# Kernel tuning notes

Measured on AMD Instinct MI355X. Metric: run time of the kernel, lower is better.

The kernel has to match this reference:

```python
import jax, jax.numpy as jnp
import numpy as np

B, S, D_MODEL, FFN, P = 8, 4096, 256, 1024, 8
BLK = 256  # token block size for the max-plus reduction


def setup_inputs() -> dict:
    key = jax.random.key(0)
    ks = jax.random.split(key, 12)
    x = jax.random.normal(ks[0], (B, S, D_MODEL), jnp.float32)
    # TropicalLinear params (additive semiring weights -> small scale)
    Wt = 0.05 * jax.random.normal(ks[1], (FFN, D_MODEL), jnp.float32)
    bt = 0.05 * jax.random.normal(ks[2], (FFN,), jnp.float32)
    # LFDualActivation: per-channel piecewise-linear convex (max) and concave (min)
    # branches, blended by a per-channel sigmoid gate alpha ('blend' mode).
    sl_cvx = 1.0 + 0.1 * jax.random.normal(ks[3], (FFN, P), jnp.float32)
    of_cvx = 0.1 * jax.random.normal(ks[4], (FFN, P), jnp.float32)
    sl_ccv = 1.0 + 0.1 * jax.random.normal(ks[5], (FFN, P), jnp.float32)
    of_ccv = 0.1 * jax.random.normal(ks[6], (FFN, P), jnp.float32)
    alpha = jnp.zeros((FFN,), jnp.float32)
    # Classical branch
    Wc = jax.random.normal(ks[7], (D_MODEL, FFN), jnp.float32) / np.sqrt(D_MODEL)
    bc = jnp.zeros((FFN,), jnp.float32)
    # Gate: init per source (weight ~0, bias +2.0 -> g ~ 0.88 tropical)
    Wg = 0.01 * jax.random.normal(ks[8], (D_MODEL, FFN), jnp.float32)
    bg = 2.0 * jnp.ones((FFN,), jnp.float32)
    # Down projection
    Wd = jax.random.normal(ks[9], (FFN, D_MODEL), jnp.float32) / np.sqrt(FFN)
    bd = jnp.zeros((D_MODEL,), jnp.float32)
    return {"x": x, "Wt": Wt, "bt": bt, "sl_cvx": sl_cvx, "of_cvx": of_cvx,
            "sl_ccv": sl_ccv, "of_ccv": of_ccv, "alpha": alpha,
            "Wc": Wc, "bc": bc, "Wg": Wg, "bg": bg, "Wd": Wd, "bd": bd}


def reference(x, Wt, bt, sl_cvx, of_cvx, sl_ccv, of_ccv, alpha, Wc, bc, Wg, bg, Wd, bd):
    Bx, Sx, D = x.shape
    T = Bx * Sx
    xf = x.reshape(T, D)
    xb = xf.reshape(T // BLK, BLK, D)
    s = jax.nn.sigmoid(alpha)  # [FFN]

    def blk_fn(xx):  # xx: [BLK, D]
        # Tropical (max-plus) linear: t[n,m] = max_k(xx[n,k] + Wt[m,k]) + bt[m]
        t = jnp.max(xx[:, None, :] + Wt[None, :, :], axis=-1) + bt  # [BLK, FFN]
        # LF dual activation: blend of convex (max of lines) and concave (min of lines)
        z = t[:, :, None]  # [BLK, FFN, 1]
        cvx = jnp.max(z * sl_cvx[None] + of_cvx[None], axis=-1)
        ccv = jnp.min(z * sl_ccv[None] + of_ccv[None], axis=-1)
        return s * cvx + (1.0 - s) * ccv  # [BLK, FFN]

    trop = jax.lax.map(blk_fn, xb).reshape(T, FFN)  # dropout = identity (eval)
    classical = jax.nn.gelu(xf @ Wc + bc, approximate=False)
    g = jax.nn.sigmoid(xf @ Wg + bg)
    fused = g * trop + (1.0 - g) * classical
    out = fused @ Wd + bd  # final dropout = identity (eval)
    return out.reshape(Bx, Sx, D)
```

## Files before the change

kernel.cpp:

```cpp
#include <hip/hip_runtime.h>

#define TTOK 32768
#define DM   256
#define NF   1024
#define KMAX 32

typedef __attribute__((ext_vector_type(8))) unsigned short ushort8;
typedef __attribute__((ext_vector_type(8))) __bf16 bf16x8;
typedef __attribute__((ext_vector_type(4))) float floatx4;

constexpr size_t O_SLOT = 0;
constexpr size_t O_S    = 256;
constexpr size_t O_WCT  = O_S    + 4096;
constexpr size_t O_WGT  = O_WCT  + (size_t)NF*DM*2;
constexpr size_t O_WDT  = O_WGT  + (size_t)NF*DM*2;
constexpr size_t O_WTT  = O_WDT  + (size_t)DM*NF*2;
constexpr size_t O_XBF  = O_WTT  + (size_t)DM*NF*4;
constexpr size_t O_CNT  = O_XBF  + (size_t)TTOK*DM*2;
constexpr size_t O_CIDX = O_CNT  + (size_t)TTOK*4;
constexpr size_t O_CVAL = O_CIDX + (size_t)TTOK*KMAX*4;
constexpr size_t O_FUSD = O_CVAL + (size_t)TTOK*KMAX*4;

__device__ __forceinline__ float bf2f(unsigned short u) {
    union { unsigned int i; float f; } c; c.i = ((unsigned int)u) << 16; return c.f;
}
__device__ __forceinline__ unsigned short f2bf(float v) {
    union { float f; unsigned int i; } c; c.f = v;
    unsigned int b = c.i;
    return (unsigned short)((b + 0x7FFFu + ((b >> 16) & 1u)) >> 16);
}
__device__ __forceinline__ float sigm(float z) { return 1.0f / (1.0f + __expf(-z)); }
__device__ __forceinline__ float gelu_f(float x) {
    return x * sigm(1.59576912f * (x + 0.044715f * x * x * x));
}
__device__ __forceinline__ void g2lds16(const unsigned short* g, unsigned short* l) {
    __builtin_amdgcn_global_load_lds((const __attribute__((address_space(1))) unsigned int*)g,
                                     (__attribute__((address_space(3))) unsigned int*)l, 16, 0, 0);
}

__global__ void pack_kernel(const float* __restrict__ Wt, const float* __restrict__ alpha,
                            const float* __restrict__ Wc, const float* __restrict__ Wg,
                            const float* __restrict__ Wd,
                            unsigned short* __restrict__ Wct, unsigned short* __restrict__ Wgt,
                            unsigned short* __restrict__ WdT, float* __restrict__ WtT,
                            float* __restrict__ s, unsigned int* __restrict__ slot) {
    int e = blockIdx.x * 256 + threadIdx.x;
    if (e == 0) *slot = 0u;
    { int f = e >> 8, k = e & 255;
      Wct[e] = f2bf(Wc[k * NF + f]);
      Wgt[e] = f2bf(Wg[k * NF + f]); }
    { int n = e >> 10, k = e & 1023;
      WdT[e] = f2bf(Wd[k * DM + n]); }
    { int d = e >> 10, f = e & 1023;
      WtT[e] = Wt[f * DM + d]; }
    if (e < NF) s[e] = sigm(alpha[e]);
}

__global__ void minmax_kernel(const float* __restrict__ Wt, unsigned int* __restrict__ slot) {
    int g = blockIdx.x * 256 + threadIdx.x;
    float lm = 0.0f;
    for (int i = g; i < NF * DM; i += 128 * 256) lm = fmaxf(lm, fabsf(Wt[i]));
    #pragma unroll
    for (int o = 32; o > 0; o >>= 1) lm = fmaxf(lm, __shfl_xor(lm, o));
    if ((threadIdx.x & 63) == 0) atomicMax(slot, __float_as_uint(lm));
}

__global__ void cand_kernel(const float* __restrict__ x, const unsigned int* __restrict__ slot,
                            unsigned short* __restrict__ xbf, int* __restrict__ counts,
                            int* __restrict__ cidx, float* __restrict__ cval) {
    int i = blockIdx.x, t = threadIdx.x;
    float v = x[i * DM + t];
    xbf[i * DM + t] = f2bf(v);
    float m = v;
    #pragma unroll
    for (int o = 32; o > 0; o >>= 1) m = fmaxf(m, __shfl_xor(m, o));
    __shared__ float wm[4];
    __shared__ int cnt;
    __shared__ int sidx[KMAX];
    __shared__ float sval[KMAX];
    if ((t & 63) == 0) wm[t >> 6] = m;
    if (t == 0) cnt = 0;
    __syncthreads();
    float xmax = fmaxf(fmaxf(wm[0], wm[1]), fmaxf(wm[2], wm[3]));
    float delta = 2.0f * __uint_as_float(*slot);
    float thr = xmax - delta;
    if (v >= thr) {
        int p = atomicAdd(&cnt, 1);
        if (p < KMAX) { sidx[p] = t; sval[p] = v; }
    }
    __syncthreads();
    int c = cnt;
    if (t == 0) counts[i] = c;
    if (t < (c < KMAX ? c : KMAX)) {
        cidx[i * KMAX + t] = sidx[t];
        cval[i * KMAX + t] = sval[t];
    }
}

#define LDSS 32
#define KPAD 33
#define OSTR 136
__global__ __launch_bounds__(512, 4) void gemm1_kernel(
    const unsigned short* __restrict__ A,
    const unsigned short* __restrict__ Bct,
    const unsigned short* __restrict__ Bgt,
    const float* __restrict__ bc, const float* __restrict__ bg,
    const int* __restrict__ counts, const int* __restrict__ cidx,
    const float* __restrict__ cval, const float* __restrict__ x,
    const float* __restrict__ WtT, const float* __restrict__ bt,
    const float* __restrict__ slx, const float* __restrict__ ofx,
    const float* __restrict__ slc, const float* __restrict__ ofc,
    const float* __restrict__ s, unsigned short* __restrict__ fused) {
    __shared__ __align__(16) char smem[76800];
    unsigned short* As  = (unsigned short*)smem;
    unsigned short* Bcs = As + 4096;
    unsigned short* Bgs = As + 8192;
    float* par = (float*)smem;
    int* sOV  = (int*)(smem + 24576);
    int* sCnt = (int*)(smem + 41472);
    unsigned short* obuf = (unsigned short*)(smem + 41984);
    const int t = threadIdx.x;
    const int b = blockIdx.x;
    const int xcd = b & 7, j = b >> 3;
    const int bf = j & 7;
    const int bm = (j >> 3) * 8 + xcd;
    const int wave = t >> 6, lane = t & 63;
    const int wm = wave & 1, wn = wave >> 1;
    const int lr = lane & 15, quad = lane >> 4;
    const int srow = wave * 16 + (lane >> 2), scol = (lane & 3) << 3;
    const unsigned short* gA = A   + (size_t)(bm * 128 + srow) * DM + scol;
    const unsigned short* gC = Bct + (size_t)(bf * 128 + srow) * DM + scol;
    const unsigned short* gG = Bgt + (size_t)(bf * 128 + srow) * DM + scol;
    unsigned short* lA = &As[wave * 16 * LDSS];
    unsigned short* lC = &Bcs[wave * 16 * LDSS];
    unsigned short* lG = &Bgs[wave * 16 * LDSS];

    if (t < 128) sCnt[t] = counts[bm * 128 + t];

    floatx4 accc[4][2], accg[4][2];
    #pragma unroll
    for (int i = 0; i < 4; i++)
        #pragma unroll
        for (int jj = 0; jj < 2; jj++) { accc[i][jj] = (floatx4)0.0f; accg[i][jj] = (floatx4)0.0f; }

    for (int k0 = 0; k0 < DM; k0 += 32) {
        __syncthreads();
        g2lds16(gA + k0, lA);
        g2lds16(gC + k0, lC);
        g2lds16(gG + k0, lG);
        __syncthreads();
        bf16x8 af[4], bcf[2], bgf[2];
        #pragma unroll
        for (int mi = 0; mi < 4; mi++)
            af[mi] = *(const bf16x8*)&As[(wm * 64 + mi * 16 + lr) * LDSS + quad * 8];
        #pragma unroll
        for (int ni = 0; ni < 2; ni++) {
            bcf[ni] = *(const bf16x8*)&Bcs[(wn * 32 + ni * 16 + lr) * LDSS + quad * 8];
            bgf[ni] = *(const bf16x8*)&Bgs[(wn * 32 + ni * 16 + lr) * LDSS + quad * 8];
        }
        #pragma unroll
        for (int mi = 0; mi < 4; mi++)
            #pragma unroll
            for (int ni = 0; ni < 2; ni++) {
                accc[mi][ni] = __builtin_amdgcn_mfma_f32_16x16x32_bf16(af[mi], bcf[ni], accc[mi][ni], 0, 0, 0);
                accg[mi][ni] = __builtin_amdgcn_mfma_f32_16x16x32_bf16(af[mi], bgf[ni], accg[mi][ni], 0, 0, 0);
            }
    }
    __syncthreads();

    for (int e = t; e < 1024; e += 512) {
        int ff = e >> 3, w = e & 7;
        int gf = (bf * 128 + ff) * 8 + w;
        par[ff * 36 + w]      = slx[gf];
        par[ff * 36 + 8 + w]  = ofx[gf];
        par[ff * 36 + 16 + w] = slc[gf];
        par[ff * 36 + 24 + w] = ofc[gf];
    }
    if (t < 128) {
        int gf = bf * 128 + t;
        par[t * 36 + 32] = bt[gf];
        par[t * 36 + 33] = s[gf];
        par[t * 36 + 34] = bc[gf];
        par[t * 36 + 35] = bg[gf];
    }
    const int PADV = (int)(((unsigned int)f2bf(-1e30f)) << 16);
    for (int e = t; e < 128 * KMAX; e += 512) {
        int m = e >> 5, k = e & 31;
        int c = sCnt[m];
        int pk = PADV;
        if (k < (c < KMAX ? c : KMAX)) {
            int d  = cidx[(size_t)(bm * 128 + m) * KMAX + k];
            float v = cval[(size_t)(bm * 128 + m) * KMAX + k];
            pk = (int)(((unsigned int)f2bf(v)) << 16) | d;
        }
        sOV[m * KPAD + k] = pk;
    }
    __syncthreads();

    const int f0 = bf * 128 + wn * 32 + lr;
    #pragma unroll
    for (int mi = 0; mi < 4; mi++) {
        const int mb = wm * 64 + mi * 16 + quad * 4;
        int c0 = sCnt[mb], c1 = sCnt[mb + 1], c2 = sCnt[mb + 2], c3 = sCnt[mb + 3];
        int k0c = c0 < KMAX ? c0 : KMAX, k1c = c1 < KMAX ? c1 : KMAX;
        int k2c = c2 < KMAX ? c2 : KMAX, k3c = c3 < KMAX ? c3 : KMAX;
        int km = max(max(k0c, k1c), max(k2c, k3c));
        float z0a = -1e30f, z1a = -1e30f, z2a = -1e30f, z3a = -1e30f;
        float z0b = -1e30f, z1b = -1e30f, z2b = -1e30f, z3b = -1e30f;
        for (int k = 0; k < km; k++) {
            int p0 = sOV[(mb + 0) * KPAD + k];
            int p1 = sOV[(mb + 1) * KPAD + k];
            int p2 = sOV[(mb + 2) * KPAD + k];
            int p3 = sOV[(mb + 3) * KPAD + k];
            const float* r0 = WtT + ((p0 & 0xFFFF) << 10) + f0;
            const float* r1 = WtT + ((p1 & 0xFFFF) << 10) + f0;
            const float* r2 = WtT + ((p2 & 0xFFFF) << 10) + f0;
            const float* r3 = WtT + ((p3 & 0xFFFF) << 10) + f0;
            float w0a = r0[0], w0b = r0[16];
            float w1a = r1[0], w1b = r1[16];
            float w2a = r2[0], w2b = r2[16];
            float w3a = r3[0], w3b = r3[16];
            float v0 = __int_as_float(p0 & 0xFFFF0000);
            float v1 = __int_as_float(p1 & 0xFFFF0000);
            float v2 = __int_as_float(p2 & 0xFFFF0000);
            float v3 = __int_as_float(p3 & 0xFFFF0000);
            z0a = fmaxf(z0a, v0 + w0a); z0b = fmaxf(z0b, v0 + w0b);
            z1a = fmaxf(z1a, v1 + w1a); z1b = fmaxf(z1b, v1 + w1b);
            z2a = fmaxf(z2a, v2 + w2a); z2b = fmaxf(z2b, v2 + w2b);
            z3a = fmaxf(z3a, v3 + w3a); z3b = fmaxf(z3b, v3 + w3b);
        }
        if (c0 > KMAX || c1 > KMAX || c2 > KMAX || c3 > KMAX) {
            float za[4] = { z0a, z1a, z2a, z3a };
            float zb[4] = { z0b, z1b, z2b, z3b };
            int cc[4] = { c0, c1, c2, c3 };
            #pragma unroll 1
            for (int r = 0; r < 4; r++) if (cc[r] > KMAX) {
                const float* xr = x + (size_t)(bm * 128 + mb + r) * DM;
                float ma = -1e30f, mbv = -1e30f;
                for (int d = 0; d < DM; d++) {
                    float xv = xr[d];
                    ma  = fmaxf(ma,  xv + WtT[d * NF + f0]);
                    mbv = fmaxf(mbv, xv + WtT[d * NF + f0 + 16]);
                }
                za[r] = ma; zb[r] = mbv;
            }
            z0a = za[0]; z1a = za[1]; z2a = za[2]; z3a = za[3];
            z0b = zb[0]; z1b = zb[1]; z2b = zb[2]; z3b = zb[3];
        }
        #pragma unroll
        for (int ni = 0; ni < 2; ni++) {
            const int fl = wn * 32 + ni * 16 + lr;
            const float* pp = par + fl * 36;
            float4 a0 = *(const float4*)(pp),      a1 = *(const float4*)(pp + 4);
            float4 b0 = *(const float4*)(pp + 8),  b1 = *(const float4*)(pp + 12);
            float4 cc0 = *(const float4*)(pp + 16), cc1 = *(const float4*)(pp + 20);
            float4 d0 = *(const float4*)(pp + 24), d1 = *(const float4*)(pp + 28);
            float4 sc = *(const float4*)(pp + 32);
            float zr[4];
            if (ni == 0) { zr[0] = z0a; zr[1] = z1a; zr[2] = z2a; zr[3] = z3a; }
            else         { zr[0] = z0b; zr[1] = z1b; zr[2] = z2b; zr[3] = z3b; }
            #pragma unroll
            for (int r = 0; r < 4; r++) {
                float z = zr[r] + sc.x;
                float cvx = fmaf(z, a0.x, b0.x);
                cvx = fmaxf(cvx, fmaf(z, a0.y, b0.y));
                cvx = fmaxf(cvx, fmaf(z, a0.z, b0.z));
                cvx = fmaxf(cvx, fmaf(z, a0.w, b0.w));
                cvx = fmaxf(cvx, fmaf(z, a1.x, b1.x));
                cvx = fmaxf(cvx, fmaf(z, a1.y, b1.y));
                cvx = fmaxf(cvx, fmaf(z, a1.z, b1.z));
                cvx = fmaxf(cvx, fmaf(z, a1.w, b1.w));
                float ccv = fmaf(z, cc0.x, d0.x);
                ccv = fminf(ccv, fmaf(z, cc0.y, d0.y));
                ccv = fminf(ccv, fmaf(z, cc0.z, d0.z));
                ccv = fminf(ccv, fmaf(z, cc0.w, d0.w));
                ccv = fminf(ccv, fmaf(z, cc1.x, d1.x));
                ccv = fminf(ccv, fmaf(z, cc1.y, d1.y));
                ccv = fminf(ccv, fmaf(z, cc1.z, d1.z));
                ccv = fminf(ccv, fmaf(z, cc1.w, d1.w));
                float tv = sc.y * cvx + (1.0f - sc.y) * ccv;
                float cpre = accc[mi][ni][r] + sc.z;
                float gpre = accg[mi][ni][r] + sc.w;
                float g = sigm(gpre);
                float cla = gelu_f(cpre);
                obuf[(mb + r) * OSTR + fl] = f2bf(g * tv + (1.0f - g) * cla);
            }
        }
    }
    __syncthreads();
    #pragma unroll
    for (int e = t; e < 128 * 16; e += 512) {
        int row = e >> 4, c8 = (e & 15) << 3;
        ushort8 v = *(const ushort8*)&obuf[row * OSTR + c8];
        *(ushort8*)&fused[(size_t)(bm * 128 + row) * NF + bf * 128 + c8] = v;
    }
}

#define LDS2 64
__global__ __launch_bounds__(512, 4) void gemm2_kernel(
    const unsigned short* __restrict__ A,
    const unsigned short* __restrict__ Bt,
    const float* __restrict__ bd, float* __restrict__ out) {
    __shared__ __align__(16) unsigned short As[128 * LDS2];
    __shared__ __align__(16) unsigned short Bs[128 * LDS2];
    const int t = threadIdx.x;
    const int b = blockIdx.x;
    const int xcd = b & 7, j = b >> 3;
    const int bn = j & 1;
    const int bm = (j >> 1) * 8 + xcd;
    const int wave = t >> 6, lane = t & 63;
    const int wm = wave & 1, wn = wave >> 1;
    const int lr = lane & 15, quad = lane >> 4;
    const int srow = wave * 8 + (lane >> 3), scol = (lane & 7) << 3;
    const unsigned short* gA = A  + (size_t)(bm * 128 + srow) * NF + scol;
    const unsigned short* gB = Bt + (size_t)(bn * 128 + srow) * NF + scol;
    unsigned short* lA = &As[wave * 8 * LDS2];
    unsigned short* lB = &Bs[wave * 8 * LDS2];

    floatx4 acc[4][2];
    #pragma unroll
    for (int i = 0; i < 4; i++)
        #pragma unroll
        for (int jj = 0; jj < 2; jj++) acc[i][jj] = (floatx4)0.0f;

    for (int k0 = 0; k0 < NF; k0 += 64) {
        __syncthreads();
        g2lds16(gA + k0, lA);
        g2lds16(gA + k0 + (size_t)64 * NF, lA + 64 * LDS2);
        g2lds16(gB + k0, lB);
        g2lds16(gB + k0 + (size_t)64 * NF, lB + 64 * LDS2);
        __syncthreads();
        #pragma unroll
        for (int ks = 0; ks < 2; ks++) {
            bf16x8 af[4], bf_[2];
            #pragma unroll
            for (int mi = 0; mi < 4; mi++)
                af[mi] = *(const bf16x8*)&As[(wm * 64 + mi * 16 + lr) * LDS2 + ks * 32 + quad * 8];
            #pragma unroll
            for (int ni = 0; ni < 2; ni++)
                bf_[ni] = *(const bf16x8*)&Bs[(wn * 32 + ni * 16 + lr) * LDS2 + ks * 32 + quad * 8];
            #pragma unroll
            for (int mi = 0; mi < 4; mi++)
                #pragma unroll
                for (int ni = 0; ni < 2; ni++)
                    acc[mi][ni] = __builtin_amdgcn_mfma_f32_16x16x32_bf16(af[mi], bf_[ni], acc[mi][ni], 0, 0, 0);
        }
    }
    #pragma unroll
    for (int mi = 0; mi < 4; mi++)
        #pragma unroll
        for (int ni = 0; ni < 2; ni++) {
            int n = bn * 128 + wn * 32 + ni * 16 + lr;
            float bdv = bd[n];
            #pragma unroll
            for (int r = 0; r < 4; r++) {
                int m = bm * 128 + wm * 64 + mi * 16 + quad * 4 + r;
                out[m * DM + n] = acc[mi][ni][r] + bdv;
            }
        }
}

extern "C" void kernel_launch(void* const* d_in, const int* in_sizes, int n_in,
                              void* d_out, int out_size, void* d_ws, size_t ws_size,
                              hipStream_t stream) {
    const float* x     = (const float*)d_in[0];
    const float* Wt    = (const float*)d_in[1];
    const float* bt    = (const float*)d_in[2];
    const float* slx   = (const float*)d_in[3];
    const float* ofx   = (const float*)d_in[4];
    const float* slc   = (const float*)d_in[5];
    const float* ofc   = (const float*)d_in[6];
    const float* alpha = (const float*)d_in[7];
    const float* Wc    = (const float*)d_in[8];
    const float* bc    = (const float*)d_in[9];
    const float* Wg    = (const float*)d_in[10];
    const float* bg    = (const float*)d_in[11];
    const float* Wd    = (const float*)d_in[12];
    const float* bd    = (const float*)d_in[13];
    float* out = (float*)d_out;
    char* ws = (char*)d_ws;

    unsigned int* slot = (unsigned int*)(ws + O_SLOT);
    float* s           = (float*)(ws + O_S);
    unsigned short* Wct = (unsigned short*)(ws + O_WCT);
    unsigned short* Wgt = (unsigned short*)(ws + O_WGT);
    unsigned short* WdT = (unsigned short*)(ws + O_WDT);
    float* WtT          = (float*)(ws + O_WTT);
    unsigned short* xbf = (unsigned short*)(ws + O_XBF);
    int* counts         = (int*)(ws + O_CNT);
    int* cidx           = (int*)(ws + O_CIDX);
    float* cval         = (float*)(ws + O_CVAL);
    unsigned short* fused = (unsigned short*)(ws + O_FUSD);

    pack_kernel<<<1024, 256, 0, stream>>>(Wt, alpha, Wc, Wg, Wd, Wct, Wgt, WdT, WtT, s, slot);
    minmax_kernel<<<128, 256, 0, stream>>>(Wt, slot);
    cand_kernel<<<TTOK, 256, 0, stream>>>(x, slot, xbf, counts, cidx, cval);
    gemm1_kernel<<<2048, 512, 0, stream>>>(
        xbf, Wct, Wgt, bc, bg, counts, cidx, cval, x, WtT, bt,
        slx, ofx, slc, ofc, s, fused);
    gemm2_kernel<<<512, 512, 0, stream>>>(fused, WdT, bd, out);
}
```

Measured before the change: 286.6 us.

## Shrink gemm1 tile to 128x64, cut LDS, cap candidates, per-wave output stores

The fused first GEMM now uses 128x64 output tiles and launches twice as many blocks. Its LDS footprint drops from about 75 KB to 31 KB, and launch bounds are raised to 6 blocks per CU to get more occupancy. The candidate list kept in LDS is capped at 12 entries and loaded before the GEMM loop. Any row with more candidates falls back to the exact full max-plus scan. Output is staged per wave with an XOR swizzle and written directly, which removes the final block-wide barrier, at the cost of reloading A tiles twice as often.

```diff
diff --git a/kernel.cpp b/kernel.cpp
--- a/kernel.cpp
+++ b/kernel.cpp
@@ -97,10 +97,10 @@
     }
 }
 
-#define LDSS 32
-#define KPAD 33
-#define OSTR 136
-__global__ __launch_bounds__(512, 4) void gemm1_kernel(
+#define LDSS  32
+#define KCAP  12
+#define KPADL 13
+__global__ __launch_bounds__(512, 6) void gemm1_kernel(
     const unsigned short* __restrict__ A,
     const unsigned short* __restrict__ Bct,
     const unsigned short* __restrict__ Bgt,
@@ -111,55 +111,68 @@
     const float* __restrict__ slx, const float* __restrict__ ofx,
     const float* __restrict__ slc, const float* __restrict__ ofc,
     const float* __restrict__ s, unsigned short* __restrict__ fused) {
-    __shared__ __align__(16) char smem[76800];
+    __shared__ __align__(16) char smem[31744];
     unsigned short* As  = (unsigned short*)smem;
     unsigned short* Bcs = As + 4096;
-    unsigned short* Bgs = As + 8192;
+    unsigned short* Bgs = As + 6144;
     float* par = (float*)smem;
+    unsigned short* obuf = (unsigned short*)(smem + 16384);
     int* sOV  = (int*)(smem + 24576);
-    int* sCnt = (int*)(smem + 41472);
-    unsigned short* obuf = (unsigned short*)(smem + 41984);
+    int* sCnt = (int*)(smem + 31232);
     const int t = threadIdx.x;
     const int b = blockIdx.x;
     const int xcd = b & 7, j = b >> 3;
-    const int bf = j & 7;
-    const int bm = (j >> 3) * 8 + xcd;
+    const int bfb = j & 15;
+    const int bm  = (j >> 4) * 8 + xcd;
     const int wave = t >> 6, lane = t & 63;
-    const int wm = wave & 1, wn = wave >> 1;
+    const int wm = wave >> 1, wf = wave & 1;
     const int lr = lane & 15, quad = lane >> 4;
-    const int srow = wave * 16 + (lane >> 2), scol = (lane & 3) << 3;
-    const unsigned short* gA = A   + (size_t)(bm * 128 + srow) * DM + scol;
-    const unsigned short* gC = Bct + (size_t)(bf * 128 + srow) * DM + scol;
-    const unsigned short* gG = Bgt + (size_t)(bf * 128 + srow) * DM + scol;
-    unsigned short* lA = &As[wave * 16 * LDSS];
-    unsigned short* lC = &Bcs[wave * 16 * LDSS];
-    unsigned short* lG = &Bgs[wave * 16 * LDSS];
 
     if (t < 128) sCnt[t] = counts[bm * 128 + t];
-
-    floatx4 accc[4][2], accg[4][2];
-    #pragma unroll
-    for (int i = 0; i < 4; i++)
+    const int PADV = (int)(((unsigned int)f2bf(-1e30f)) << 16);
+    for (int e = t; e < 2048; e += 512) {
+        int m = e >> 4, k = e & 15;
+        if (k < KCAP) {
+            int c = counts[bm * 128 + m];
+            int pk = PADV;
+            if (k < (c < KCAP ? c : KCAP)) {
+                int d  = cidx[(size_t)(bm * 128 + m) * KMAX + k];
+                float v = cval[(size_t)(bm * 128 + m) * KMAX + k];
+                pk = (int)(((unsigned int)f2bf(v)) << 16) | d;
+            }
+            sOV[m * KPADL + k] = pk;
+        }
+    }
+
+    const unsigned short* gbase;
+    unsigned short* lbase;
+    if (wave < 4)      { gbase = A   + (size_t)(bm * 128 + wave * 32) * DM;       lbase = &As[wave * 32 * LDSS]; }
+    else if (wave < 6) { gbase = Bct + (size_t)(bfb * 64 + (wave - 4) * 32) * DM; lbase = &Bcs[(wave - 4) * 32 * LDSS]; }
+    else               { gbase = Bgt + (size_t)(bfb * 64 + (wave - 6) * 32) * DM; lbase = &Bgs[(wave - 6) * 32 * LDSS]; }
+    const unsigned short* g0 = gbase + (size_t)(lane >> 2) * DM + ((lane & 3) << 3);
+
+    floatx4 accc[2][2], accg[2][2];
+    #pragma unroll
+    for (int i = 0; i < 2; i++)
         #pragma unroll
         for (int jj = 0; jj < 2; jj++) { accc[i][jj] = (floatx4)0.0f; accg[i][jj] = (floatx4)0.0f; }
 
     for (int k0 = 0; k0 < DM; k0 += 32) {
         __syncthreads();
-        g2lds16(gA + k0, lA);
-        g2lds16(gC + k0, lC);
-        g2lds16(gG + k0, lG);
+        g2lds16(g0 + k0, lbase);
+        g2lds16(g0 + 16 * DM + k0, lbase + 16 * LDSS);
         __syncthreads();
-        bf16x8 af[4], bcf[2], bgf[2];
-        #pragma unroll
-        for (int mi = 0; mi < 4; mi++)
-            af[mi] = *(const bf16x8*)&As[(wm * 64 + mi * 16 + lr) * LDSS + quad * 8];
+        bf16x8 af[2], bcf[2], bgf[2];
+        #pragma unroll
+        for (int mi = 0; mi < 2; mi++)
+            af[mi] = *(const bf16x8*)&As[(wm * 32 + mi * 16 + lr) * LDSS + quad * 8];
         #pragma unroll
         for (int ni = 0; ni < 2; ni++) {
-            bcf[ni] = *(const bf16x8*)&Bcs[(wn * 32 + ni * 16 + lr) * LDSS + quad * 8];
-            bgf[ni] = *(const bf16x8*)&Bgs[(wn * 32 + ni * 16 + lr) * LDSS + quad * 8];
-        }
-        #pragma unroll
-        for (int mi = 0; mi < 4; mi++)
+            bcf[ni] = *(const bf16x8*)&Bcs[(wf * 32 + ni * 16 + lr) * LDSS + quad * 8];
+            bgf[ni] = *(const bf16x8*)&Bgs[(wf * 32 + ni * 16 + lr) * LDSS + quad * 8];
+        }
+        #pragma unroll
+        for (int mi = 0; mi < 2; mi++)
             #pragma unroll
             for (int ni = 0; ni < 2; ni++) {
                 accc[mi][ni] = __builtin_amdgcn_mfma_f32_16x16x32_bf16(af[mi], bcf[ni], accc[mi][ni], 0, 0, 0);
@@ -168,50 +181,37 @@
     }
     __syncthreads();
 
-    for (int e = t; e < 1024; e += 512) {
-        int ff = e >> 3, w = e & 7;
-        int gf = (bf * 128 + ff) * 8 + w;
-        par[ff * 36 + w]      = slx[gf];
-        par[ff * 36 + 8 + w]  = ofx[gf];
-        par[ff * 36 + 16 + w] = slc[gf];
-        par[ff * 36 + 24 + w] = ofc[gf];
-    }
-    if (t < 128) {
-        int gf = bf * 128 + t;
+    { int ff = t >> 3, w = t & 7;
+      int gf = (bfb * 64 + ff) * 8 + w;
+      par[ff * 36 + w]      = slx[gf];
+      par[ff * 36 + 8 + w]  = ofx[gf];
+      par[ff * 36 + 16 + w] = slc[gf];
+      par[ff * 36 + 24 + w] = ofc[gf]; }
+    if (t < 64) {
+        int gf = bfb * 64 + t;
         par[t * 36 + 32] = bt[gf];
         par[t * 36 + 33] = s[gf];
         par[t * 36 + 34] = bc[gf];
         par[t * 36 + 35] = bg[gf];
     }
-    const int PADV = (int)(((unsigned int)f2bf(-1e30f)) << 16);
-    for (int e = t; e < 128 * KMAX; e += 512) {
-        int m = e >> 5, k = e & 31;
-        int c = sCnt[m];
-        int pk = PADV;
-        if (k < (c < KMAX ? c : KMAX)) {
-            int d  = cidx[(size_t)(bm * 128 + m) * KMAX + k];
-            float v = cval[(size_t)(bm * 128 + m) * KMAX + k];
-            pk = (int)(((unsigned int)f2bf(v)) << 16) | d;
-        }
-        sOV[m * KPAD + k] = pk;
-    }
     __syncthreads();
 
-    const int f0 = bf * 128 + wn * 32 + lr;
-    #pragma unroll
-    for (int mi = 0; mi < 4; mi++) {
-        const int mb = wm * 64 + mi * 16 + quad * 4;
+    const int f0 = bfb * 64 + wf * 32 + lr;
+    unsigned short* owave = obuf + wave * 512;
+    #pragma unroll
+    for (int mi = 0; mi < 2; mi++) {
+        const int mb = wm * 32 + mi * 16 + quad * 4;
         int c0 = sCnt[mb], c1 = sCnt[mb + 1], c2 = sCnt[mb + 2], c3 = sCnt[mb + 3];
-        int k0c = c0 < KMAX ? c0 : KMAX, k1c = c1 < KMAX ? c1 : KMAX;
-        int k2c = c2 < KMAX ? c2 : KMAX, k3c = c3 < KMAX ? c3 : KMAX;
+        int k0c = c0 < KCAP ? c0 : KCAP, k1c = c1 < KCAP ? c1 : KCAP;
+        int k2c = c2 < KCAP ? c2 : KCAP, k3c = c3 < KCAP ? c3 : KCAP;
         int km = max(max(k0c, k1c), max(k2c, k3c));
         float z0a = -1e30f, z1a = -1e30f, z2a = -1e30f, z3a = -1e30f;
         float z0b = -1e30f, z1b = -1e30f, z2b = -1e30f, z3b = -1e30f;
         for (int k = 0; k < km; k++) {
-            int p0 = sOV[(mb + 0) * KPAD + k];
-            int p1 = sOV[(mb + 1) * KPAD + k];
-            int p2 = sOV[(mb + 2) * KPAD + k];
-            int p3 = sOV[(mb + 3) * KPAD + k];
+            int p0 = sOV[(mb + 0) * KPADL + k];
+            int p1 = sOV[(mb + 1) * KPADL + k];
+            int p2 = sOV[(mb + 2) * KPADL + k];
+            int p3 = sOV[(mb + 3) * KPADL + k];
             const float* r0 = WtT + ((p0 & 0xFFFF) << 10) + f0;
             const float* r1 = WtT + ((p1 & 0xFFFF) << 10) + f0;
             const float* r2 = WtT + ((p2 & 0xFFFF) << 10) + f0;
@@ -229,12 +229,12 @@
             z2a = fmaxf(z2a, v2 + w2a); z2b = fmaxf(z2b, v2 + w2b);
             z3a = fmaxf(z3a, v3 + w3a); z3b = fmaxf(z3b, v3 + w3b);
         }
-        if (c0 > KMAX || c1 > KMAX || c2 > KMAX || c3 > KMAX) {
+        if (c0 > KCAP || c1 > KCAP || c2 > KCAP || c3 > KCAP) {
             float za[4] = { z0a, z1a, z2a, z3a };
             float zb[4] = { z0b, z1b, z2b, z3b };
             int cc[4] = { c0, c1, c2, c3 };
             #pragma unroll 1
-            for (int r = 0; r < 4; r++) if (cc[r] > KMAX) {
+            for (int r = 0; r < 4; r++) if (cc[r] > KCAP) {
                 const float* xr = x + (size_t)(bm * 128 + mb + r) * DM;
                 float ma = -1e30f, mbv = -1e30f;
                 for (int d = 0; d < DM; d++) {
@@ -249,7 +249,7 @@
         }
         #pragma unroll
         for (int ni = 0; ni < 2; ni++) {
-            const int fl = wn * 32 + ni * 16 + lr;
+            const int fl = wf * 32 + ni * 16 + lr;
             const float* pp = par + fl * 36;
             float4 a0 = *(const float4*)(pp),      a1 = *(const float4*)(pp + 4);
             float4 b0 = *(const float4*)(pp + 8),  b1 = *(const float4*)(pp + 12);
@@ -283,16 +283,16 @@
                 float gpre = accg[mi][ni][r] + sc.w;
                 float g = sigm(gpre);
                 float cla = gelu_f(cpre);
-                obuf[(mb + r) * OSTR + fl] = f2bf(g * tv + (1.0f - g) * cla);
+                int row = quad * 4 + r;
+                owave[row * 32 + ((ni * 16 + lr) ^ (quad << 3))] = f2bf(g * tv + (1.0f - g) * cla);
             }
         }
-    }
-    __syncthreads();
-    #pragma unroll
-    for (int e = t; e < 128 * 16; e += 512) {
-        int row = e >> 4, c8 = (e & 15) << 3;
-        ushort8 v = *(const ushort8*)&obuf[row * OSTR + c8];
-        *(ushort8*)&fused[(size_t)(bm * 128 + row) * NF + bf * 128 + c8] = v;
+        {
+            int rl = lane >> 2, ch = lane & 3;
+            ushort8 v = *(const ushort8*)&owave[rl * 32 + ((ch ^ (rl >> 2)) << 3)];
+            *(ushort8*)&fused[(size_t)(bm * 128 + wm * 32 + mi * 16 + rl) * NF
+                              + bfb * 64 + wf * 32 + ch * 8] = v;
+        }
     }
 }
 
@@ -395,7 +395,7 @@
     pack_kernel<<<1024, 256, 0, stream>>>(Wt, alpha, Wc, Wg, Wd, Wct, Wgt, WdT, WtT, s, slot);
     minmax_kernel<<<128, 256, 0, stream>>>(Wt, slot);
     cand_kernel<<<TTOK, 256, 0, stream>>>(x, slot, xbf, counts, cidx, cval);
-    gemm1_kernel<<<2048, 512, 0, stream>>>(
+    gemm1_kernel<<<4096, 512, 0, stream>>>(
         xbf, Wct, Wgt, bc, bg, counts, cidx, cval, x, WtT, bt,
         slx, ofx, slc, ofc, s, fused);
     gemm2_kernel<<<512, 512, 0, stream>>>(fused, WdT, bd, out);
```

Result: slower. 495.2 us (+72.8%).

## Double-buffer GEMM1 K-loop, use wave-per-token candidate selection, cap candidates

Applied to the files above, without the earlier changes.

The candidate kernel now gives each token to a single wavefront and compacts candidates with ballot/popcount instead of shared-memory atomics and block barriers, so a launch has a quarter as many blocks. In gemm1, the shared-memory layout is reorganised so the candidate and parameter staging happens before the MFMA loop, and that loop double-buffers its LDS tiles so the next K slice loads while the current one computes. The per-token candidate cap used in gemm1 drops from 32 to 16, which sends more tokens to the slow full-scan fallback if they have many candidates.

```diff
diff --git a/kernel.cpp b/kernel.cpp
--- a/kernel.cpp
+++ b/kernel.cpp
@@ -65,41 +65,47 @@
     if ((threadIdx.x & 63) == 0) atomicMax(slot, __float_as_uint(lm));
 }
 
-__global__ void cand_kernel(const float* __restrict__ x, const unsigned int* __restrict__ slot,
-                            unsigned short* __restrict__ xbf, int* __restrict__ counts,
-                            int* __restrict__ cidx, float* __restrict__ cval) {
-    int i = blockIdx.x, t = threadIdx.x;
-    float v = x[i * DM + t];
-    xbf[i * DM + t] = f2bf(v);
-    float m = v;
+__global__ __launch_bounds__(256) void cand_kernel(
+        const float* __restrict__ x, const unsigned int* __restrict__ slot,
+        unsigned short* __restrict__ xbf, int* __restrict__ counts,
+        int* __restrict__ cidx, float* __restrict__ cval) {
+    const int wave = threadIdx.x >> 6, lane = threadIdx.x & 63;
+    const int tok = blockIdx.x * 4 + wave;
+    const float* xr = x + (size_t)tok * DM;
+    float v0 = xr[lane], v1 = xr[lane + 64], v2 = xr[lane + 128], v3 = xr[lane + 192];
+    unsigned short* xo = xbf + (size_t)tok * DM;
+    xo[lane]       = f2bf(v0);
+    xo[lane + 64]  = f2bf(v1);
+    xo[lane + 128] = f2bf(v2);
+    xo[lane + 192] = f2bf(v3);
+    float m = fmaxf(fmaxf(v0, v1), fmaxf(v2, v3));
     #pragma unroll
     for (int o = 32; o > 0; o >>= 1) m = fmaxf(m, __shfl_xor(m, o));
-    __shared__ float wm[4];
-    __shared__ int cnt;
-    __shared__ int sidx[KMAX];
-    __shared__ float sval[KMAX];
-    if ((t & 63) == 0) wm[t >> 6] = m;
-    if (t == 0) cnt = 0;
-    __syncthreads();
-    float xmax = fmaxf(fmaxf(wm[0], wm[1]), fmaxf(wm[2], wm[3]));
-    float delta = 2.0f * __uint_as_float(*slot);
-    float thr = xmax - delta;
-    if (v >= thr) {
-        int p = atomicAdd(&cnt, 1);
-        if (p < KMAX) { sidx[p] = t; sval[p] = v; }
-    }
-    __syncthreads();
-    int c = cnt;
-    if (t == 0) counts[i] = c;
-    if (t < (c < KMAX ? c : KMAX)) {
-        cidx[i * KMAX + t] = sidx[t];
-        cval[i * KMAX + t] = sval[t];
-    }
-}
-
-#define LDSS 32
-#define KPAD 33
-#define OSTR 136
+    const float delta = 2.0f * __uint_as_float(*slot);
+    const float thr = m - delta;
+    const unsigned long long lt = (lane == 63) ? 0x7FFFFFFFFFFFFFFFull
+                                               : ((1ull << lane) - 1ull);
+    float vv[4] = { v0, v1, v2, v3 };
+    int base = 0;
+    #pragma unroll
+    for (int j = 0; j < 4; j++) {
+        bool p = vv[j] >= thr;
+        unsigned long long mask = __ballot(p);
+        int pos = base + __popcll(mask & lt);
+        if (p && pos < KMAX) {
+            cidx[(size_t)tok * KMAX + pos] = lane + j * 64;
+            cval[(size_t)tok * KMAX + pos] = vv[j];
+        }
+        base += __popcll(mask);
+    }
+    if (lane == 0) counts[tok] = base;
+}
+
+#define LDSS  32
+#define KCAP  16
+#define KPADL 17
+#define OSTR  136
+#define STAGEB 24576
 __global__ __launch_bounds__(512, 4) void gemm1_kernel(
     const unsigned short* __restrict__ A,
     const unsigned short* __restrict__ Bct,
@@ -112,13 +118,10 @@
     const float* __restrict__ slc, const float* __restrict__ ofc,
     const float* __restrict__ s, unsigned short* __restrict__ fused) {
     __shared__ __align__(16) char smem[76800];
-    unsigned short* As  = (unsigned short*)smem;
-    unsigned short* Bcs = As + 4096;
-    unsigned short* Bgs = As + 8192;
-    float* par = (float*)smem;
-    int* sOV  = (int*)(smem + 24576);
-    int* sCnt = (int*)(smem + 41472);
-    unsigned short* obuf = (unsigned short*)(smem + 41984);
+    unsigned short* obuf = (unsigned short*)smem;
+    float* par = (float*)(smem + 49152);
+    int* sOV  = (int*)(smem + 67584);
+    int* sCnt = (int*)(smem + 76288);
     const int t = threadIdx.x;
     const int b = blockIdx.x;
     const int xcd = b & 7, j = b >> 3;
@@ -131,43 +134,23 @@
     const unsigned short* gA = A   + (size_t)(bm * 128 + srow) * DM + scol;
     const unsigned short* gC = Bct + (size_t)(bf * 128 + srow) * DM + scol;
     const unsigned short* gG = Bgt + (size_t)(bf * 128 + srow) * DM + scol;
-    unsigned short* lA = &As[wave * 16 * LDSS];
-    unsigned short* lC = &Bcs[wave * 16 * LDSS];
-    unsigned short* lG = &Bgs[wave * 16 * LDSS];
+    const int lofs = wave * 16 * LDSS;
 
     if (t < 128) sCnt[t] = counts[bm * 128 + t];
-
-    floatx4 accc[4][2], accg[4][2];
-    #pragma unroll
-    for (int i = 0; i < 4; i++)
-        #pragma unroll
-        for (int jj = 0; jj < 2; jj++) { accc[i][jj] = (floatx4)0.0f; accg[i][jj] = (floatx4)0.0f; }
-
-    for (int k0 = 0; k0 < DM; k0 += 32) {
-        __syncthreads();
-        g2lds16(gA + k0, lA);
-        g2lds16(gC + k0, lC);
-        g2lds16(gG + k0, lG);
-        __syncthreads();
-        bf16x8 af[4], bcf[2], bgf[2];
-        #pragma unroll
-        for (int mi = 0; mi < 4; mi++)
-            af[mi] = *(const bf16x8*)&As[(wm * 64 + mi * 16 + lr) * LDSS + quad * 8];
-        #pragma unroll
-        for (int ni = 0; ni < 2; ni++) {
-            bcf[ni] = *(const bf16x8*)&Bcs[(wn * 32 + ni * 16 + lr) * LDSS + quad * 8];
-            bgf[ni] = *(const bf16x8*)&Bgs[(wn * 32 + ni * 16 + lr) * LDSS + quad * 8];
-        }
-        #pragma unroll
-        for (int mi = 0; mi < 4; mi++)
-            #pragma unroll
-            for (int ni = 0; ni < 2; ni++) {
-                accc[mi][ni] = __builtin_amdgcn_mfma_f32_16x16x32_bf16(af[mi], bcf[ni], accc[mi][ni], 0, 0, 0);
-                accg[mi][ni] = __builtin_amdgcn_mfma_f32_16x16x32_bf16(af[mi], bgf[ni], accg[mi][ni], 0, 0, 0);
-            }
-    }
-    __syncthreads();
-
+    const int PADV = (int)(((unsigned int)f2bf(-1e30f)) << 16);
+    #pragma unroll
+    for (int e = t; e < 2048; e += 512) {
+        int m = e >> 4, k = e & 15;
+        int c = counts[bm * 128 + m];
+        int pk = PADV;
+        if (k < (c < KCAP ? c : KCAP)) {
+            int d  = cidx[(size_t)(bm * 128 + m) * KMAX + k];
+            float v = cval[(size_t)(bm * 128 + m) * KMAX + k];
+            pk = (int)(((unsigned int)f2bf(v)) << 16) | d;
+        }
+        sOV[m * KPADL + k] = pk;
+    }
+    #pragma unroll
     for (int e = t; e < 1024; e += 512) {
         int ff = e >> 3, w = e & 7;
         int gf = (bf * 128 + ff) * 8 + w;
@@ -183,35 +166,64 @@
         par[t * 36 + 34] = bc[gf];
         par[t * 36 + 35] = bg[gf];
     }
-    const int PADV = (int)(((unsigned int)f2bf(-1e30f)) << 16);
-    for (int e = t; e < 128 * KMAX; e += 512) {
-        int m = e >> 5, k = e & 31;
-        int c = sCnt[m];
-        int pk = PADV;
-        if (k < (c < KMAX ? c : KMAX)) {
-            int d  = cidx[(size_t)(bm * 128 + m) * KMAX + k];
-            float v = cval[(size_t)(bm * 128 + m) * KMAX + k];
-            pk = (int)(((unsigned int)f2bf(v)) << 16) | d;
-        }
-        sOV[m * KPAD + k] = pk;
+
+    floatx4 accc[4][2], accg[4][2];
+    #pragma unroll
+    for (int i = 0; i < 4; i++)
+        #pragma unroll
+        for (int jj = 0; jj < 2; jj++) { accc[i][jj] = (floatx4)0.0f; accg[i][jj] = (floatx4)0.0f; }
+
+    {
+        unsigned short* b0 = (unsigned short*)smem;
+        g2lds16(gA, b0 + lofs);
+        g2lds16(gC, b0 + 4096 + lofs);
+        g2lds16(gG, b0 + 8192 + lofs);
     }
     __syncthreads();
+    #pragma unroll
+    for (int k = 0; k < 8; k++) {
+        unsigned short* cur = (unsigned short*)(smem + (size_t)(k & 1) * STAGEB);
+        if (k < 7) {
+            unsigned short* nxt = (unsigned short*)(smem + (size_t)((k + 1) & 1) * STAGEB);
+            int k0 = (k + 1) * 32;
+            g2lds16(gA + k0, nxt + lofs);
+            g2lds16(gC + k0, nxt + 4096 + lofs);
+            g2lds16(gG + k0, nxt + 8192 + lofs);
+        }
+        bf16x8 af[4], bcf[2], bgf[2];
+        #pragma unroll
+        for (int mi = 0; mi < 4; mi++)
+            af[mi] = *(const bf16x8*)&cur[(wm * 64 + mi * 16 + lr) * LDSS + quad * 8];
+        #pragma unroll
+        for (int ni = 0; ni < 2; ni++) {
+            bcf[ni] = *(const bf16x8*)&cur[4096 + (wn * 32 + ni * 16 + lr) * LDSS + quad * 8];
+            bgf[ni] = *(const bf16x8*)&cur[8192 + (wn * 32 + ni * 16 + lr) * LDSS + quad * 8];
+        }
+        #pragma unroll
+        for (int mi = 0; mi < 4; mi++)
+            #pragma unroll
+            for (int ni = 0; ni < 2; ni++) {
+                accc[mi][ni] = __builtin_amdgcn_mfma_f32_16x16x32_bf16(af[mi], bcf[ni], accc[mi][ni], 0, 0, 0);
+                accg[mi][ni] = __builtin_amdgcn_mfma_f32_16x16x32_bf16(af[mi], bgf[ni], accg[mi][ni], 0, 0, 0);
+            }
+        __syncthreads();
+    }
 
     const int f0 = bf * 128 + wn * 32 + lr;
     #pragma unroll
     for (int mi = 0; mi < 4; mi++) {
         const int mb = wm * 64 + mi * 16 + quad * 4;
         int c0 = sCnt[mb], c1 = sCnt[mb + 1], c2 = sCnt[mb + 2], c3 = sCnt[mb + 3];
-        int k0c = c0 < KMAX ? c0 : KMAX, k1c = c1 < KMAX ? c1 : KMAX;
-        int k2c = c2 < KMAX ? c2 : KMAX, k3c = c3 < KMAX ? c3 : KMAX;
+        int k0c = c0 < KCAP ? c0 : KCAP, k1c = c1 < KCAP ? c1 : KCAP;
+        int k2c = c2 < KCAP ? c2 : KCAP, k3c = c3 < KCAP ? c3 : KCAP;
         int km = max(max(k0c, k1c), max(k2c, k3c));
         float z0a = -1e30f, z1a = -1e30f, z2a = -1e30f, z3a = -1e30f;
         float z0b = -1e30f, z1b = -1e30f, z2b = -1e30f, z3b = -1e30f;
         for (int k = 0; k < km; k++) {
-            int p0 = sOV[(mb + 0) * KPAD + k];
-            int p1 = sOV[(mb + 1) * KPAD + k];
-            int p2 = sOV[(mb + 2) * KPAD + k];
-            int p3 = sOV[(mb + 3) * KPAD + k];
+            int p0 = sOV[(mb + 0) * KPADL + k];
+            int p1 = sOV[(mb + 1) * KPADL + k];
+            int p2 = sOV[(mb + 2) * KPADL + k];
+            int p3 = sOV[(mb + 3) * KPADL + k];
             const float* r0 = WtT + ((p0 & 0xFFFF) << 10) + f0;
             const float* r1 = WtT + ((p1 & 0xFFFF) << 10) + f0;
             const float* r2 = WtT + ((p2 & 0xFFFF) << 10) + f0;
@@ -229,12 +241,12 @@
             z2a = fmaxf(z2a, v2 + w2a); z2b = fmaxf(z2b, v2 + w2b);
             z3a = fmaxf(z3a, v3 + w3a); z3b = fmaxf(z3b, v3 + w3b);
         }
-        if (c0 > KMAX || c1 > KMAX || c2 > KMAX || c3 > KMAX) {
+        if (c0 > KCAP || c1 > KCAP || c2 > KCAP || c3 > KCAP) {
             float za[4] = { z0a, z1a, z2a, z3a };
             float zb[4] = { z0b, z1b, z2b, z3b };
             int cc[4] = { c0, c1, c2, c3 };
             #pragma unroll 1
-            for (int r = 0; r < 4; r++) if (cc[r] > KMAX) {
+            for (int r = 0; r < 4; r++) if (cc[r] > KCAP) {
                 const float* xr = x + (size_t)(bm * 128 + mb + r) * DM;
                 float ma = -1e30f, mbv = -1e30f;
                 for (int d = 0; d < DM; d++) {
@@ -394,7 +406,7 @@
 
     pack_kernel<<<1024, 256, 0, stream>>>(Wt, alpha, Wc, Wg, Wd, Wct, Wgt, WdT, WtT, s, slot);
     minmax_kernel<<<128, 256, 0, stream>>>(Wt, slot);
-    cand_kernel<<<TTOK, 256, 0, stream>>>(x, slot, xbf, counts, cidx, cval);
+    cand_kernel<<<TTOK / 4, 256, 0, stream>>>(x, slot, xbf, counts, cidx, cval);
     gemm1_kernel<<<2048, 512, 0, stream>>>(
         xbf, Wct, Wgt, bc, bg, counts, cidx, cval, x, WtT, bt,
         slx, ofx, slc, ofc, s, fused);
```

Measured after the change: 328.5 us. +14.6%, slower.
